# Kernel tuning notes

Measured on AMD Instinct MI355X. Metric: run time of the kernel, lower is better.

Reference implementation:

```python
import jax, jax.numpy as jnp
import numpy as np

N, F_IN, T, E, O = 50000, 32, 8, 800000, 32


def setup_inputs() -> dict:
    ks = jax.random.split(jax.random.key(0), 16)
    s = 0.05
    return {
        "X": jax.random.normal(ks[0], (N, F_IN, T), dtype=jnp.float32),
        "edge_index": jax.random.randint(ks[1], (2, E), 0, N, dtype=jnp.int64),
        "edge_weight": jax.random.uniform(ks[2], (E,), dtype=jnp.float32),
        # GCNConv weights for z/r/h gates: lin weight [O, F_IN], bias [O]
        "Wz": jax.random.normal(ks[3], (O, F_IN), dtype=jnp.float32) * s,
        "bz": jnp.zeros((O,), dtype=jnp.float32),
        "Wr": jax.random.normal(ks[4], (O, F_IN), dtype=jnp.float32) * s,
        "br": jnp.zeros((O,), dtype=jnp.float32),
        "Wh": jax.random.normal(ks[5], (O, F_IN), dtype=jnp.float32) * s,
        "bh": jnp.zeros((O,), dtype=jnp.float32),
        # Linear(2*O, O) per gate
        "Lz": jax.random.normal(ks[6], (O, 2 * O), dtype=jnp.float32) * s,
        "lz_b": jnp.zeros((O,), dtype=jnp.float32),
        "Lr": jax.random.normal(ks[7], (O, 2 * O), dtype=jnp.float32) * s,
        "lr_b": jnp.ones((O,), dtype=jnp.float32),
        "Lh": jax.random.normal(ks[8], (O, 2 * O), dtype=jnp.float32) * s,
        "lh_b": jnp.zeros((O,), dtype=jnp.float32),
        "attention": jax.random.uniform(ks[9], (T,), dtype=jnp.float32),
    }


def reference(X, edge_index, edge_weight, Wz, bz, Wr, br, Wh, bh,
              Lz, lz_b, Lr, lr_b, Lh, lh_b, attention):
    n = X.shape[0]
    # --- GCN normalization with self-loops (computed once; graph is static) ---
    loop = jnp.arange(n, dtype=edge_index.dtype)
    row = jnp.concatenate([edge_index[0], loop])
    col = jnp.concatenate([edge_index[1], loop])
    ew = jnp.concatenate([edge_weight, jnp.ones((n,), dtype=X.dtype)])
    deg = jax.ops.segment_sum(ew, col, num_segments=n)
    deg_safe = jnp.where(deg > 0, deg, 1.0)
    dinv = jnp.where(deg > 0, jax.lax.rsqrt(deg_safe), 0.0)
    norm = dinv[row] * ew * dinv[col]  # [E+N]

    def conv(x, W, b):
        h = x @ W.T                                   # [N, O]
        msg = norm[:, None] * h[row]                  # gather over sources
        return jax.ops.segment_sum(msg, col, num_segments=n) + b

    def tgcn_cell(x, H):
        Z = jax.nn.sigmoid(jnp.concatenate([conv(x, Wz, bz), H], axis=1) @ Lz.T + lz_b)
        R = jax.nn.sigmoid(jnp.concatenate([conv(x, Wr, br), H], axis=1) @ Lr.T + lr_b)
        H_tilde = jnp.tanh(jnp.concatenate([conv(x, Wh, bh), H * R], axis=1) @ Lh.T + lh_b)
        return Z * H + (1.0 - Z) * H_tilde

    H0 = jnp.zeros((n, Lz.shape[0]), dtype=X.dtype)   # hidden init (H=None)
    probs = jax.nn.softmax(attention)
    Xs = jnp.moveaxis(X, 2, 0)                        # [T, N, F]

    def step(acc, inp):
        x_t, p = inp
        return acc + p * tgcn_cell(x_t, H0), None

    H_accum, _ = jax.lax.scan(step, H0, (Xs, probs))
    return H_accum
```

## Files before the change

kernel.cpp:

```cpp
#include <hip/hip_runtime.h>
#include <hip/hip_fp16.h>
#include <math.h>


#define GATH16(EV, WT)                                                     \
  {                                                                        \
    unsigned voff = ((unsigned)(EV) << 9) | loff;                          \
    uint2 q = *(const uint2*)((const char*)Xh + voff);                     \
    __half2 ha = *(__half2*)&q.x;                                          \
    __half2 hb = *(__half2*)&q.y;                                          \
    acc.x = fmaf((WT), __low2float(ha),  acc.x);                           \
    acc.y = fmaf((WT), __high2float(ha), acc.y);                           \
    acc.z = fmaf((WT), __low2float(hb),  acc.z);                           \
    acc.w = fmaf((WT), __high2float(hb), acc.w);                           \
  }

__device__ inline void do_prep(int g, int tid,
    const float* __restrict__ Wz, const float* __restrict__ bz,
    const float* __restrict__ Wh, const float* __restrict__ bh,
    const float* __restrict__ Lz, const float* __restrict__ lzb,
    const float* __restrict__ Lh, const float* __restrict__ lhb,
    const float* __restrict__ att,
    float* __restrict__ Mt, float* __restrict__ cvec, float* __restrict__ p) {
  const float* L  = g ? Lh  : Lz;
  const float* W  = g ? Wh  : Wz;
  const float* bb = g ? bh  : bz;
  const float* lb = g ? lhb : lzb;
  int o = tid & 31;
  for (int f = tid >> 5; f < 32; f += 8) {
    float s = 0.f;
    for (int k = 0; k < 32; ++k) s += L[o * 64 + k] * W[k * 32 + f];
    Mt[g * 1024 + f * 32 + o] = s;
  }
  if (tid < 32) {
    float c = lb[tid];
    for (int k = 0; k < 32; ++k) c += L[tid * 64 + k] * bb[k];
    cvec[g * 32 + tid] = c;
  }
  if (g == 0 && tid == 0) {
    float m = att[0];
    for (int t = 1; t < 8; ++t) m = fmaxf(m, att[t]);
    float e8[8], sm = 0.f;
    for (int t = 0; t < 8; ++t) { e8[t] = expf(att[t] - m); sm += e8[t]; }
    for (int t = 0; t < 8; ++t) p[t] = e8[t] / sm;
  }
}

__global__ __launch_bounds__(256) void k1_part(
    const int* __restrict__ ei, const float* __restrict__ ew,
    unsigned long long* __restrict__ pk, int2* __restrict__ slot, int cap,
    const float* __restrict__ Wz, const float* __restrict__ bz,
    const float* __restrict__ Wh, const float* __restrict__ bh,
    const float* __restrict__ Lz, const float* __restrict__ lzb,
    const float* __restrict__ Lh, const float* __restrict__ lhb,
    const float* __restrict__ att,
    float* __restrict__ Mt, float* __restrict__ cvec, float* __restrict__ p,
    int E, int N, int K) {
  int b = blockIdx.x;
  int tid = threadIdx.x;
  int nedge = K << 3;
  if (b >= nedge) {
    do_prep(b - nedge, tid, Wz, bz, Wh, bh, Lz, lzb, Lh, lhb, att, Mt, cvec, p);
    return;
  }
  int g = b & 7;
  int n = b >> 3;
  int slice = (N + 7) >> 3;
  int lo = g * slice;
  int hi = lo + slice; if (hi > N) hi = N;
  int stride = K << 8;
  for (int e = (n << 8) + tid; e < E; e += stride) {
    int c = ei[E + e];
    if (c >= lo && c < hi) {
      int r = ei[e];
      float w = ew[e];
      unsigned wfx = (unsigned)(w * 16777216.0f + 0.5f);
      unsigned long long old =
          atomicAdd(pk + c, ((unsigned long long)wfx << 32) | 1ull);
      unsigned pos = (unsigned)(old & 0xffffffffull);
      if (pos < (unsigned)cap)
        slot[(size_t)c * cap + pos] = make_int2(r, __float_as_int(w));
    }
  }
}

__global__ __launch_bounds__(256) void k2_conv(
    const float* __restrict__ X, const unsigned long long* __restrict__ pk,
    __half* __restrict__ Xh, long n8) {
  long i = blockIdx.x * (long)blockDim.x + threadIdx.x;
  if (i < n8) {
    int node = (int)(i >> 5);
    unsigned long long v = pk[node];
    float di = rsqrtf((float)(v >> 32) * (1.0f / 16777216.0f) + 1.0f);
    const float4* Xv = (const float4*)X;
    float4 a = Xv[2 * i], c = Xv[2 * i + 1];
    union { int4 i4; __half2 h[4]; } u;
    u.h[0] = __floats2half2_rn(di * a.x, di * a.y);
    u.h[1] = __floats2half2_rn(di * a.z, di * a.w);
    u.h[2] = __floats2half2_rn(di * c.x, di * c.y);
    u.h[3] = __floats2half2_rn(di * c.z, di * c.w);
    ((int4*)Xh)[i] = u.i4;
  }
}

__global__ __launch_bounds__(64) void k3_main(
    const __half* __restrict__ Xh, const unsigned long long* __restrict__ pk,
    const int2* __restrict__ slot, int cap,
    const float* __restrict__ Mt, const float* __restrict__ cvec,
    const float* __restrict__ p, float* __restrict__ out) {
  int node = blockIdx.x;
  int l = threadIdx.x;
  __shared__ float ax[256];

  unsigned long long v = pk[node];
  int cnt = (int)(v & 0xffffffffull);
  if (cnt > cap) cnt = cap;
  float di = rsqrtf((float)(v >> 32) * (1.0f / 16777216.0f) + 1.0f);

  float4 acc = make_float4(0.f, 0.f, 0.f, 0.f);
  unsigned loff = (unsigned)l << 3;

  GATH16(node, 1.0f);
  const int2* row = slot + (size_t)node * cap;
  int j = 0;
  for (; j + 7 < cnt; j += 8) {
    int2 e0 = row[j],     e1 = row[j + 1], e2 = row[j + 2], e3 = row[j + 3];
    int2 e4 = row[j + 4], e5 = row[j + 5], e6 = row[j + 6], e7 = row[j + 7];
    GATH16(e0.x, __int_as_float(e0.y));
    GATH16(e1.x, __int_as_float(e1.y));
    GATH16(e2.x, __int_as_float(e2.y));
    GATH16(e3.x, __int_as_float(e3.y));
    GATH16(e4.x, __int_as_float(e4.y));
    GATH16(e5.x, __int_as_float(e5.y));
    GATH16(e6.x, __int_as_float(e6.y));
    GATH16(e7.x, __int_as_float(e7.y));
  }
  for (; j < cnt; ++j) {
    int2 e0 = row[j];
    GATH16(e0.x, __int_as_float(e0.y));
  }
  acc.x *= di; acc.y *= di; acc.z *= di; acc.w *= di;

  ((float4*)ax)[l] = acc;
  __syncthreads();

  int o = l & 31, g = l >> 5;
  float c = cvec[g * 32 + o];
  float pre[8];
#pragma unroll
  for (int t = 0; t < 8; ++t) pre[t] = c;

  const float*  M   = Mt + g * 1024;
  const float4* axv = (const float4*)ax;
#pragma unroll 8
  for (int f = 0; f < 32; ++f) {
    float  m  = M[f * 32 + o];
    float4 a0 = axv[f * 2];
    float4 a1 = axv[f * 2 + 1];
    pre[0] = fmaf(m, a0.x, pre[0]); pre[1] = fmaf(m, a0.y, pre[1]);
    pre[2] = fmaf(m, a0.z, pre[2]); pre[3] = fmaf(m, a0.w, pre[3]);
    pre[4] = fmaf(m, a1.x, pre[4]); pre[5] = fmaf(m, a1.y, pre[5]);
    pre[6] = fmaf(m, a1.z, pre[6]); pre[7] = fmaf(m, a1.w, pre[7]);
  }

  float vv[8];
  if (g == 0) {
#pragma unroll
    for (int t = 0; t < 8; ++t)
      vv[t] = __builtin_amdgcn_rcpf(1.f + __expf(pre[t]));
  } else {
#pragma unroll
    for (int t = 0; t < 8; ++t)
      vv[t] = 1.f - 2.f * __builtin_amdgcn_rcpf(__expf(2.f * pre[t]) + 1.f);
  }

  float res = 0.f;
#pragma unroll
  for (int t = 0; t < 8; ++t) {
    float other = __shfl(vv[t], l ^ 32);
    res += p[t] * vv[t] * other;
  }
  if (g == 0) out[(size_t)node * 32 + o] = res;
}


extern "C" void kernel_launch(void* const* d_in, const int* in_sizes, int n_in,
                              void* d_out, int out_size, void* d_ws, size_t ws_size,
                              hipStream_t stream) {
  const float* X   = (const float*)d_in[0];
  const int*   ei  = (const int*)d_in[1];
  const float* ew  = (const float*)d_in[2];
  const float* Wz  = (const float*)d_in[3];
  const float* bz  = (const float*)d_in[4];
  const float* Wh  = (const float*)d_in[7];
  const float* bh  = (const float*)d_in[8];
  const float* Lz  = (const float*)d_in[9];
  const float* lzb = (const float*)d_in[10];
  const float* Lh  = (const float*)d_in[13];
  const float* lhb = (const float*)d_in[14];
  const float* att = (const float*)d_in[15];

  int N = in_sizes[0] / 256;
  int E = in_sizes[2];
  (void)n_in; (void)out_size;

  long n8  = (long)N * 32;
  int  nbc = (int)((n8 + 255) / 256);
  int  K   = (E + 2047) / 2048;

  size_t off = 0;
  auto al = [&](size_t b) { size_t q = off; off = (off + b + 255) & ~(size_t)255; return q; };
  size_t o_pk  = al((size_t)N * 8);
  size_t o_mt  = al(2048 * 4);
  size_t o_cv  = al(64 * 4);
  size_t o_p   = al(8 * 4);
  size_t o_xh  = al((size_t)N * 256 * 2);
  size_t fixed = off;
  int cap = 0;
  for (int c : {64, 48, 32}) {
    if (fixed + (size_t)N * c * 8 <= ws_size) { cap = c; break; }
  }
  if (!cap) return;

  char* w = (char*)d_ws;
  unsigned long long* pk = (unsigned long long*)(w + o_pk);
  float* Mt   = (float*)(w + o_mt);
  float* cvec = (float*)(w + o_cv);
  float* p    = (float*)(w + o_p);
  __half* Xh  = (__half*)(w + o_xh);
  int2*  slot = (int2*)(w + fixed);

  (void)hipMemsetAsync(pk, 0, (size_t)N * 8, stream);
  k1_part<<<K * 8 + 2, 256, 0, stream>>>(ei, ew, pk, slot, cap,
                                         Wz, bz, Wh, bh, Lz, lzb, Lh, lhb,
                                         att, Mt, cvec, p, E, N, K);
  k2_conv<<<nbc, 256, 0, stream>>>(X, pk, Xh, n8);
  k3_main<<<N, 64, 0, stream>>>(Xh, pk, slot, cap, Mt, cvec, p,
                                (float*)d_out);
}
```

Baseline: 126.5 us.

## Bucket edges by destination slice before atomic slot insertion

Replaces the edge partition kernel, in which every block scanned all edges and filtered by destination slice, with a two-pass scheme. The first pass reads each edge once and appends a packed record to one of eight per-slice segments, using shared-memory counters and one global atomic per slice per block. The second pass walks each segment and does the per-node atomic insertion. The pk zeroing also moves into the first kernel in place of a separate memset of that array. This removes the eightfold redundant reads of the edge list, at the cost of an extra kernel launch, an intermediate buffer, and packing limits of 17 bits for the source index and 15 bits for the slice offset.

```diff
diff --git a/kernel.cpp b/kernel.cpp
--- a/kernel.cpp
+++ b/kernel.cpp
@@ -46,41 +46,89 @@
   }
 }
 
-__global__ __launch_bounds__(256) void k1_part(
+__global__ __launch_bounds__(256) void k0(
     const int* __restrict__ ei, const float* __restrict__ ew,
-    unsigned long long* __restrict__ pk, int2* __restrict__ slot, int cap,
+    unsigned long long* __restrict__ pk, int N2,
+    unsigned long long* __restrict__ seg, int segcap, int* __restrict__ cur8,
+    int slice, unsigned long long Mdiv,
     const float* __restrict__ Wz, const float* __restrict__ bz,
     const float* __restrict__ Wh, const float* __restrict__ bh,
     const float* __restrict__ Lz, const float* __restrict__ lzb,
     const float* __restrict__ Lh, const float* __restrict__ lhb,
     const float* __restrict__ att,
     float* __restrict__ Mt, float* __restrict__ cvec, float* __restrict__ p,
-    int E, int N, int K) {
+    int E, int nzb) {
   int b = blockIdx.x;
   int tid = threadIdx.x;
-  int nedge = K << 3;
-  if (b >= nedge) {
-    do_prep(b - nedge, tid, Wz, bz, Wh, bh, Lz, lzb, Lh, lhb, att, Mt, cvec, p);
+  if (b < nzb) {
+    int i = b * 256 + tid;
+    if (i < N2) ((ulonglong2*)pk)[i] = make_ulonglong2(0ull, 0ull);
     return;
   }
-  int g = b & 7;
-  int n = b >> 3;
-  int slice = (N + 7) >> 3;
+  b -= nzb;
+  if (b < 2) { do_prep(b, tid, Wz, bz, Wh, bh, Lz, lzb, Lh, lhb, att, Mt, cvec, p); return; }
+  b -= 2;
+
+  __shared__ int lcnt[8];
+  __shared__ int lbase[8];
+  if (tid < 8) lcnt[tid] = 0;
+  __syncthreads();
+
+  int gk[4]; int lp[4]; unsigned long long rec[4];
+  int base = b * 1024 + tid;
+#pragma unroll
+  for (int k = 0; k < 4; ++k) {
+    int e = base + k * 256;
+    gk[k] = -1;
+    if (e < E) {
+      int r = ei[e];
+      int c = ei[E + e];
+      float w = ew[e];
+      int g = (int)(((unsigned long long)(unsigned)c * Mdiv) >> 48);
+      int coff = c - g * slice;
+      gk[k] = g;
+      rec[k] = ((unsigned long long)__float_as_uint(w) << 32) |
+               ((unsigned)coff << 17) | (unsigned)r;
+      lp[k] = atomicAdd(&lcnt[g], 1);
+    }
+  }
+  __syncthreads();
+  if (tid < 8) lbase[tid] = atomicAdd(&cur8[tid], lcnt[tid]);
+  __syncthreads();
+#pragma unroll
+  for (int k = 0; k < 4; ++k) {
+    if (gk[k] >= 0) {
+      int pos = lbase[gk[k]] + lp[k];
+      if (pos < segcap)
+        seg[(size_t)gk[k] * segcap + pos] = rec[k];
+    }
+  }
+}
+
+__global__ __launch_bounds__(256) void kB(
+    const unsigned long long* __restrict__ seg, int segcap,
+    const int* __restrict__ cur8, unsigned long long* __restrict__ pk,
+    int2* __restrict__ slot, int cap, int slice, int Kb) {
+  int g = blockIdx.x & 7;
+  int n = blockIdx.x >> 3;
+  int cnt = cur8[g];
+  if (cnt > segcap) cnt = segcap;
+  const unsigned long long* s = seg + (size_t)g * segcap;
   int lo = g * slice;
-  int hi = lo + slice; if (hi > N) hi = N;
-  int stride = K << 8;
-  for (int e = (n << 8) + tid; e < E; e += stride) {
-    int c = ei[E + e];
-    if (c >= lo && c < hi) {
-      int r = ei[e];
-      float w = ew[e];
-      unsigned wfx = (unsigned)(w * 16777216.0f + 0.5f);
-      unsigned long long old =
-          atomicAdd(pk + c, ((unsigned long long)wfx << 32) | 1ull);
-      unsigned pos = (unsigned)(old & 0xffffffffull);
-      if (pos < (unsigned)cap)
-        slot[(size_t)c * cap + pos] = make_int2(r, __float_as_int(w));
-    }
+  int stride = Kb * 256;
+  for (int i = n * 256 + threadIdx.x; i < cnt; i += stride) {
+    unsigned long long rec = s[i];
+    int r    = (int)(rec & 0x1FFFFull);
+    int coff = (int)((rec >> 17) & 0x7FFFull);
+    unsigned wbits = (unsigned)(rec >> 32);
+    float w = __uint_as_float(wbits);
+    int c = lo + coff;
+    unsigned wfx = (unsigned)(w * 16777216.0f + 0.5f);
+    unsigned long long old =
+        atomicAdd(pk + c, ((unsigned long long)wfx << 32) | 1ull);
+    unsigned pos = (unsigned)(old & 0xffffffffull);
+    if (pos < (unsigned)cap)
+      slot[(size_t)c * cap + pos] = make_int2(r, (int)wbits);
   }
 }
 
@@ -204,17 +252,22 @@
   int E = in_sizes[2];
   (void)n_in; (void)out_size;
 
-  long n8  = (long)N * 32;
-  int  nbc = (int)((n8 + 255) / 256);
-  int  K   = (E + 2047) / 2048;
+  long n8    = (long)N * 32;
+  int  nbc   = (int)((n8 + 255) / 256);
+  int  slice = (N + 7) / 8;
+  unsigned long long Mdiv =
+      (unsigned long long)((((__uint128_t)1) << 48) / (unsigned)slice) + 1;
+  int  segcap = (E >> 3) + (E >> 6) + 1024;
 
   size_t off = 0;
   auto al = [&](size_t b) { size_t q = off; off = (off + b + 255) & ~(size_t)255; return q; };
-  size_t o_pk  = al((size_t)N * 8);
+  size_t o_pk  = al((size_t)N * 8 + 16);
   size_t o_mt  = al(2048 * 4);
   size_t o_cv  = al(64 * 4);
   size_t o_p   = al(8 * 4);
+  size_t o_c8  = al(64);
   size_t o_xh  = al((size_t)N * 256 * 2);
+  size_t o_sg  = al((size_t)segcap * 8 * 8);
   size_t fixed = off;
   int cap = 0;
   for (int c : {64, 48, 32}) {
@@ -223,17 +276,26 @@
   if (!cap) return;
 
   char* w = (char*)d_ws;
-  unsigned long long* pk = (unsigned long long*)(w + o_pk);
+  unsigned long long* pk  = (unsigned long long*)(w + o_pk);
   float* Mt   = (float*)(w + o_mt);
   float* cvec = (float*)(w + o_cv);
   float* p    = (float*)(w + o_p);
+  int*   cur8 = (int*)(w + o_c8);
   __half* Xh  = (__half*)(w + o_xh);
+  unsigned long long* seg = (unsigned long long*)(w + o_sg);
   int2*  slot = (int2*)(w + fixed);
 
-  (void)hipMemsetAsync(pk, 0, (size_t)N * 8, stream);
-  k1_part<<<K * 8 + 2, 256, 0, stream>>>(ei, ew, pk, slot, cap,
-                                         Wz, bz, Wh, bh, Lz, lzb, Lh, lhb,
-                                         att, Mt, cvec, p, E, N, K);
+  int N2  = (N + 1) / 2;
+  int nzb = (N2 + 255) / 256;
+  int nsp = (E + 1023) / 1024;
+  int Kb  = 64;
+
+  (void)hipMemsetAsync(cur8, 0, 64, stream);
+  k0<<<nzb + 2 + nsp, 256, 0, stream>>>(ei, ew, pk, N2, seg, segcap, cur8,
+                                        slice, Mdiv,
+                                        Wz, bz, Wh, bh, Lz, lzb, Lh, lhb,
+                                        att, Mt, cvec, p, E, nzb);
+  kB<<<Kb * 8, 256, 0, stream>>>(seg, segcap, cur8, pk, slot, cap, slice, Kb);
   k2_conv<<<nbc, 256, 0, stream>>>(X, pk, Xh, n8);
   k3_main<<<N, 64, 0, stream>>>(Xh, pk, slot, cap, Mt, cvec, p,
                                 (float*)d_out);
```

Result: slower. 136.6 us (+8.0%).
